# Kernel optimization log

Hardware: AMD Instinct MI355X
Metric: run time of the kernel (lower is better)

## Reference

```python
import jax, jax.numpy as jnp
import numpy as np

B, S, D = 2, 2048, 1024
H, KV, DH = 16, 4, 64
FI = 2816
V = 32000
NBLK = 2
NSTEPS = 3
CF = 0.67


def setup_inputs() -> dict:
    key = jax.random.key(0)
    ks = jax.random.split(key, 12)
    s = 0.02
    return {
        'input_ids': jax.random.randint(ks[0], (B, S), 0, V, dtype=jnp.int32),
        'emb': jax.random.normal(ks[1], (V, D), jnp.float32) * s,
        'Wq': jax.random.normal(ks[2], (NBLK, D, H * DH), jnp.float32) * s,
        'Wk': jax.random.normal(ks[3], (NBLK, D, KV * DH), jnp.float32) * s,
        'Wv': jax.random.normal(ks[4], (NBLK, D, KV * DH), jnp.float32) * s,
        'Wo': jax.random.normal(ks[5], (NBLK, H * DH, D), jnp.float32) * s,
        'Wg': jax.random.normal(ks[6], (NBLK, D, FI), jnp.float32) * s,
        'Wu': jax.random.normal(ks[7], (NBLK, D, FI), jnp.float32) * s,
        'Wd': jax.random.normal(ks[8], (NBLK, FI, D), jnp.float32) * s,
        'norm1': jnp.ones((NBLK, D), jnp.float32),
        'norm2': jnp.ones((NBLK, D), jnp.float32),
        'router_w': jax.random.normal(ks[9], (D, 1), jnp.float32) * s,
        'final_norm': jnp.ones((D,), jnp.float32),
        'lm_head': jax.random.normal(ks[10], (D, V), jnp.float32) * s,
    }


def rmsnorm(x, w, eps=1e-6):
    return x * jax.lax.rsqrt(jnp.mean(x * x, axis=-1, keepdims=True) + eps) * w


def rotate_half(x):
    x1, x2 = jnp.split(x, 2, axis=-1)
    return jnp.concatenate([-x2, x1], axis=-1)


def rope_tables(seq_len, dh):
    inv = 1.0 / (10000.0 ** (jnp.arange(0, dh, 2, dtype=jnp.float32) / dh))
    t = jnp.arange(seq_len, dtype=jnp.float32)
    freqs = t[:, None] * inv[None, :]                 # [S, dh/2]
    emb = jnp.concatenate([freqs, freqs], axis=-1)     # [S, dh]
    return jnp.cos(emb), jnp.sin(emb)


def shared_block(x, Wq, Wk, Wv, Wo, Wg, Wu, Wd, n1, n2):
    b, s, _ = x.shape
    h = rmsnorm(x, n1)
    q = (h @ Wq).reshape(b, s, H, DH).transpose(0, 2, 1, 3)   # bhsd
    k = (h @ Wk).reshape(b, s, KV, DH).transpose(0, 2, 1, 3)
    v = (h @ Wv).reshape(b, s, KV, DH).transpose(0, 2, 1, 3)
    cos, sin = rope_tables(s, DH)                              # [S, dh]
    q = q * cos + rotate_half(q) * sin
    k = k * cos + rotate_half(k) * sin
    k = jnp.repeat(k, H // KV, axis=1)   # repeat_interleave over head dim
    v = jnp.repeat(v, H // KV, axis=1)
    scale = 1.0 / jnp.sqrt(jnp.float32(DH))
    scores = jnp.einsum('bhqd,bhkd->bhqk', q, k) * scale
    causal = jnp.tril(jnp.ones((s, s), dtype=bool))
    scores = jnp.where(causal, scores, -jnp.inf)
    probs = jax.nn.softmax(scores, axis=-1)
    ctx = jnp.einsum('bhqk,bhkd->bhqd', probs, v)
    ctx = ctx.transpose(0, 2, 1, 3).reshape(b, s, H * DH)
    x = x + ctx @ Wo
    h2 = rmsnorm(x, n2)
    return x + (jax.nn.silu(h2 @ Wg) * (h2 @ Wu)) @ Wd


def reference(input_ids, emb, Wq, Wk, Wv, Wo, Wg, Wu, Wd, norm1, norm2,
              router_w, final_norm, lm_head):
    x = emb[input_ids]                      # [B, S, D]
    mask = jnp.ones((B, S), dtype=bool)     # all tokens active at depth 0
    aux_total = jnp.float32(0.0)
    n_active = B * S                        # static per step -> static top-k k
    for step in range(NSTEPS):
        keep = max(1, int(n_active * CF))
        if keep < n_active:
            # expert-choice router: sigmoid score, top-k over active tokens
            scores = jax.nn.sigmoid((x @ router_w)[..., 0])       # [B, S]
            flat = jnp.where(mask, scores, -jnp.inf).reshape(-1)  # [B*S]
            top_vals, top_idx = jax.lax.top_k(flat, keep)
            mask = jnp.zeros((B * S,), dtype=bool).at[top_idx].set(True).reshape(B, S)
            aux_total = aux_total + (-jnp.mean(top_vals) * 1e-3)
            n_active = keep
        blk = step % NBLK                   # 'cycle' sharing strategy
        out = shared_block(x, Wq[blk], Wk[blk], Wv[blk], Wo[blk],
                           Wg[blk], Wu[blk], Wd[blk], norm1[blk], norm2[blk])
        # only routed (active) tokens are updated at this recursion depth
        x = jnp.where(mask[..., None], out, x)
    x = rmsnorm(x, final_norm)
    logits = x @ lm_head                    # [B, S, V]
    return logits, aux_total
```

## Files before the change

### kernel.cpp

```cpp
#include <hip/hip_runtime.h>
#include <cmath>


constexpr int kB = 2, kS = 2048, kD = 1024, kH = 16, kKV = 4, kDH = 64,
              kFI = 2816, kV = 32000, kT = kB * kS;
constexpr size_t kBtOff  = 114688000;
constexpr size_t kAbfOff = 112590848;
constexpr size_t kXOff   = 108396544;
constexpr int kR1 = 3456;
constexpr int kQKV = 1536;
constexpr int kGU = 5632;

typedef __attribute__((ext_vector_type(8))) __bf16 bf16x8;
typedef __attribute__((ext_vector_type(4))) float f32x4;
typedef unsigned short u16;
typedef unsigned int u32;

__device__ inline u32 f2bf1(float f) {
  u32 u = __builtin_bit_cast(u32, f);
  return (u + 0x7FFFu + ((u >> 16) & 1u)) >> 16;
}
__device__ inline void splitbf(float v, u32& h, u32& l) {
  h = f2bf1(v);
  float hf = __builtin_bit_cast(float, h << 16);
  l = f2bf1(v - hf);
}
__device__ inline int xcd_remap(int hb, int nwg) {
  int q = nwg >> 3, r = nwg & 7;
  int xcd = hb & 7, pos = hb >> 3;
  int start = (xcd < r) ? xcd * (q + 1) : r * (q + 1) + (xcd - r) * q;
  return start + pos;
}

__device__ inline void stage_lds16(const u16* __restrict__ gbase, int K,
                                   int row0, int k0, char* ldsbase, int t) {
  int w = t >> 6, lane = t & 63;
#pragma unroll
  for (int i = 0; i < 4; ++i) {
    int wb = (w * 4 + i) * 1024;
    int L = wb + lane * 16;
    int r = L >> 7, inner = L & 127;
    int kc0 = (inner ^ ((r & 7) << 4)) >> 3;
    const u16* g = gbase + (size_t)(row0 + r) * K + k0 + kc0 * 4;
    __builtin_amdgcn_global_load_lds(
        (const __attribute__((address_space(1))) u32*)g,
        (__attribute__((address_space(3))) u32*)(ldsbase + wb), 16, 0, 0);
  }
}

__global__ __launch_bounds__(256) void tables_kernel(float* __restrict__ cosT,
                                                     float* __restrict__ sinT) {
  int tid = blockIdx.x * 256 + threadIdx.x;
  int t = tid >> 5, d = tid & 31;
  float inv = (float)pow(10000.0, -(double)d / 32.0);
  float fr = (float)t * inv;
  cosT[tid] = (float)cos((double)fr);
  sinT[tid] = (float)sin((double)fr);
}

__global__ void init_kernel(int* __restrict__ mask, float* __restrict__ aux) {
  int t = threadIdx.x;
  for (int e = t; e < kT; e += 256) mask[e] = 1;
  if (t == 0) aux[0] = 0.f;
}

__global__ __launch_bounds__(256) void embed_kernel(const int* __restrict__ ids,
    const float* __restrict__ emb, float* __restrict__ x) {
  int tid = blockIdx.x * 256 + threadIdx.x;
  int token = tid >> 8;
  int c4 = (tid & 255) << 2;
  int id = ids[token];
  *(float4*)&x[(size_t)token * kD + c4] =
      *(const float4*)&emb[(size_t)id * kD + c4];
}

__global__ __launch_bounds__(1024) void scan_kernel(const int* __restrict__ mask,
    int* __restrict__ cidx, int keep, int keepR) {
  __shared__ int sv[1024];
  int t = threadIdx.x;
  int base = t * 4;
  int loc[4];
  int c = 0;
#pragma unroll
  for (int j = 0; j < 4; ++j) { loc[j] = c; c += mask[base + j]; }
  sv[t] = c;
  __syncthreads();
  for (int off = 1; off < 1024; off <<= 1) {
    int v = (t >= off) ? sv[t - off] : 0;
    __syncthreads();
    sv[t] += v;
    __syncthreads();
  }
  int pre = (t == 0) ? 0 : sv[t - 1];
#pragma unroll
  for (int j = 0; j < 4; ++j)
    if (mask[base + j]) cidx[pre + loc[j]] = base + j;
  __syncthreads();
  for (int e = keep + t; e < keepR; e += 1024) cidx[e] = 0;
}

__global__ __launch_bounds__(256) void rmsnorm_split_kernel(
    const float* __restrict__ x, const float* __restrict__ w,
    u16* __restrict__ ohi, u16* __restrict__ olo) {
  int tok = blockIdx.x, t = threadIdx.x;
  const float* xr = x + (size_t)tok * kD;
  float4 xv = *(const float4*)&xr[t * 4];
  float s = xv.x * xv.x + xv.y * xv.y + xv.z * xv.z + xv.w * xv.w;
#pragma unroll
  for (int off = 1; off < 64; off <<= 1) s += __shfl_xor(s, off);
  __shared__ float red[4];
  if ((t & 63) == 0) red[t >> 6] = s;
  __syncthreads();
  float tot = red[0] + red[1] + red[2] + red[3];
  float sc = 1.f / sqrtf(tot * (1.f / kD) + 1e-6f);
  float4 wv = *(const float4*)&w[t * 4];
  float o0 = xv.x * sc * wv.x, o1 = xv.y * sc * wv.y;
  float o2 = xv.z * sc * wv.z, o3 = xv.w * sc * wv.w;
  u32 h0, h1, h2, h3, l0, l1, l2, l3;
  splitbf(o0, h0, l0); splitbf(o1, h1, l1);
  splitbf(o2, h2, l2); splitbf(o3, h3, l3);
  uint2 ph, pl;
  ph.x = h0 | (h1 << 16); ph.y = h2 | (h3 << 16);
  pl.x = l0 | (l1 << 16); pl.y = l2 | (l3 << 16);
  *(uint2*)&ohi[(size_t)tok * kD + t * 4] = ph;
  *(uint2*)&olo[(size_t)tok * kD + t * 4] = pl;
}

__global__ __launch_bounds__(256) void rmsnorm_split_gather(
    const float* __restrict__ x, const float* __restrict__ w,
    const int* __restrict__ cidx, u16* __restrict__ ohi, u16* __restrict__ olo) {
  int row = blockIdx.x, t = threadIdx.x;
  int tok = cidx[row];
  const float* xr = x + (size_t)tok * kD;
  float4 xv = *(const float4*)&xr[t * 4];
  float s = xv.x * xv.x + xv.y * xv.y + xv.z * xv.z + xv.w * xv.w;
#pragma unroll
  for (int off = 1; off < 64; off <<= 1) s += __shfl_xor(s, off);
  __shared__ float red[4];
  if ((t & 63) == 0) red[t >> 6] = s;
  __syncthreads();
  float tot = red[0] + red[1] + red[2] + red[3];
  float sc = 1.f / sqrtf(tot * (1.f / kD) + 1e-6f);
  float4 wv = *(const float4*)&w[t * 4];
  float o0 = xv.x * sc * wv.x, o1 = xv.y * sc * wv.y;
  float o2 = xv.z * sc * wv.z, o3 = xv.w * sc * wv.w;
  u32 h0, h1, h2, h3, l0, l1, l2, l3;
  splitbf(o0, h0, l0); splitbf(o1, h1, l1);
  splitbf(o2, h2, l2); splitbf(o3, h3, l3);
  uint2 ph, pl;
  ph.x = h0 | (h1 << 16); ph.y = h2 | (h3 << 16);
  pl.x = l0 | (l1 << 16); pl.y = l2 | (l3 << 16);
  *(uint2*)&ohi[(size_t)row * kD + t * 4] = ph;
  *(uint2*)&olo[(size_t)row * kD + t * 4] = pl;
}

__global__ __launch_bounds__(256) void finalnorm_conv(const float* __restrict__ x,
    const float* __restrict__ fnw, u16* __restrict__ Abf) {
  int tok = blockIdx.x, t = threadIdx.x;
  const float* xr = x + (size_t)tok * kD;
  float4 xv = *(const float4*)&xr[t * 4];
  float s = xv.x * xv.x + xv.y * xv.y + xv.z * xv.z + xv.w * xv.w;
#pragma unroll
  for (int off = 1; off < 64; off <<= 1) s += __shfl_xor(s, off);
  __shared__ float red[4];
  if ((t & 63) == 0) red[t >> 6] = s;
  __syncthreads();
  float tot = red[0] + red[1] + red[2] + red[3];
  float sc = 1.f / sqrtf(tot * (1.f / kD) + 1e-6f);
  float4 wv = *(const float4*)&fnw[t * 4];
  uint2 ph;
  ph.x = f2bf1(xv.x * sc * wv.x) | (f2bf1(xv.y * sc * wv.y) << 16);
  ph.y = f2bf1(xv.z * sc * wv.z) | (f2bf1(xv.w * sc * wv.w) << 16);
  *(uint2*)&Abf[(size_t)tok * kD + t * 4] = ph;
}

__global__ __launch_bounds__(64) void router_kernel(const float* __restrict__ x,
    const float* __restrict__ rw, float* __restrict__ scores) {
  int tok = blockIdx.x, lane = threadIdx.x;
  const float* xr = x + (size_t)tok * kD;
  double s = 0.0;
#pragma unroll
  for (int e = 0; e < kD / 64; ++e)
    s += (double)xr[lane + e * 64] * (double)rw[lane + e * 64];
#pragma unroll
  for (int off = 1; off < 64; off <<= 1) s += __shfl_xor(s, off);
  if (lane == 0) {
    float z = (float)s;
    scores[tok] = 1.f / (1.f + expf(-z));
  }
}

__global__ __launch_bounds__(1024) void topk_kernel(const float* __restrict__ scores,
    int* __restrict__ mask, float* __restrict__ aux, int keep) {
  __shared__ float sv[kT];
  __shared__ int si[kT];
  __shared__ float red[16];
  int t = threadIdx.x;
  for (int e = t; e < kT; e += 1024) {
    sv[e] = mask[e] ? scores[e] : -INFINITY;
    si[e] = e;
  }
  __syncthreads();
  for (int k = 2; k <= kT; k <<= 1) {
    for (int j = k >> 1; j > 0; j >>= 1) {
      for (int e = t; e < kT; e += 1024) {
        int p = e ^ j;
        if (p > e) {
          float v1 = sv[e], v2 = sv[p];
          int i1 = si[e], i2 = si[p];
          bool before = (v1 > v2) || (v1 == v2 && i1 < i2);
          bool desc = ((e & k) == 0);
          if (desc ? !before : before) {
            sv[e] = v2; sv[p] = v1; si[e] = i2; si[p] = i1;
          }
        }
      }
      __syncthreads();
    }
  }
  for (int e = t; e < kT; e += 1024) mask[si[e]] = (e < keep) ? 1 : 0;
  float ps = 0.f;
  for (int e = t; e < keep; e += 1024) ps += sv[e];
#pragma unroll
  for (int off = 1; off < 64; off <<= 1) ps += __shfl_xor(ps, off);
  if ((t & 63) == 0) red[t >> 6] = ps;
  __syncthreads();
  if (t == 0) {
    float tot = 0.f;
    for (int i = 0; i < 16; ++i) tot += red[i];
    aux[0] += -(tot / (float)keep) * 1e-3f;
  }
}

__global__ __launch_bounds__(256) void rope_split_kernel(
    const float* __restrict__ qkv,
    const float* __restrict__ cosT, const float* __restrict__ sinT,
    u16* __restrict__ Qh, u16* __restrict__ Ql,
    u16* __restrict__ Kh, u16* __restrict__ Kl) {
  int tid = blockIdx.x * 256 + threadIdx.x;
  const int QP = kT * kH * 32;
  const float* base;
  u16 *oh, *ol;
  size_t outoff;
  int token, d;
  if (tid < QP) {
    token = tid >> 9;
    int r = tid & 511;
    int hh = r >> 5; d = r & 31;
    base = qkv + (size_t)token * kQKV + hh * kDH;
    outoff = (size_t)token * (kH * kDH) + hh * kDH;
    oh = Qh; ol = Ql;
  } else {
    int p = tid - QP;
    token = p >> 7;
    int r = p & 127;
    int hh = r >> 5; d = r & 31;
    base = qkv + (size_t)token * kQKV + 1024 + hh * kDH;
    outoff = (size_t)token * (kKV * kDH) + hh * kDH;
    oh = Kh; ol = Kl;
  }
  int s = token & (kS - 1);
  float c = cosT[s * 32 + d], sn = sinT[s * 32 + d];
  float x1 = base[d], x2 = base[d + 32];
  float v1 = x1 * c - x2 * sn;
  float v2 = x2 * c + x1 * sn;
  u32 h1, l1, h2, l2;
  splitbf(v1, h1, l1);
  splitbf(v2, h2, l2);
  oh[outoff + d] = (u16)h1;      ol[outoff + d] = (u16)l1;
  oh[outoff + d + 32] = (u16)h2; ol[outoff + d + 32] = (u16)l2;
}

__global__ __launch_bounds__(256) void vtsplit_kernel(const float* __restrict__ qkv,
    u16* __restrict__ Th, u16* __restrict__ Tl) {
  int ktile = blockIdx.x, kv = blockIdx.y, b = blockIdx.z;
  __shared__ float T[64][65];
  int t = threadIdx.x;
#pragma unroll
  for (int p = 0; p < 16; ++p) {
    int idx = t + p * 256;
    int key = idx >> 6, d = idx & 63;
    T[key][d] =
        qkv[(size_t)(b * kS + ktile * 64 + key) * kQKV + 1280 + kv * kDH + d];
  }
  __syncthreads();
  int dr = t >> 2, kg = t & 3;
  size_t ob = ((size_t)(b * kKV + kv) * kDH + dr) * kS + ktile * 64 + kg * 16;
#pragma unroll
  for (int i = 0; i < 4; ++i) {
    int kk = kg * 16 + i * 4;
    u32 h0, h1, h2, h3, l0, l1, l2, l3;
    splitbf(T[kk + 0][dr], h0, l0); splitbf(T[kk + 1][dr], h1, l1);
    splitbf(T[kk + 2][dr], h2, l2); splitbf(T[kk + 3][dr], h3, l3);
    uint2 ph, pl;
    ph.x = h0 | (h1 << 16); ph.y = h2 | (h3 << 16);
    pl.x = l0 | (l1 << 16); pl.y = l2 | (l3 << 16);
    *(uint2*)&Th[ob + i * 4] = ph;
    *(uint2*)&Tl[ob + i * 4] = pl;
  }
}

__global__ __launch_bounds__(256) void attn_mfma(
    const u16* __restrict__ Qh, const u16* __restrict__ Ql,
    const u16* __restrict__ Kh2, const u16* __restrict__ Kl2,
    const u16* __restrict__ VTh, const u16* __restrict__ VTl,
    u16* __restrict__ ctxH, u16* __restrict__ ctxL) {
  int qb = (int)gridDim.x - 1 - (int)blockIdx.x;
  int q0 = qb * 64, hh = blockIdx.y, b = blockIdx.z;
  int t = threadIdx.x;
  int lane = t & 63, w = t >> 6;
  int kvh = hh >> 2;
  __shared__ __align__(16) char sQh[8192], sQl[8192];
  __shared__ __align__(16) char sKh[8192], sKl[8192];
  __shared__ __align__(16) char sVh[8192], sVl[8192];
  __shared__ __align__(16) char sPh[8192], sPl[8192];
#pragma unroll
  for (int p = 0; p < 4; ++p) {
    int idx = t + p * 256;
    int r = idx >> 4, kc = idx & 15;
    int off = r * 128 + ((kc * 8) ^ ((r & 7) << 4));
    size_t gq = (size_t)(b * kS + q0 + r) * (kH * kDH) + hh * kDH + kc * 4;
    *(uint2*)(sQh + off) = *(const uint2*)&Qh[gq];
    *(uint2*)(sQl + off) = *(const uint2*)&Ql[gq];
  }
  f32x4 ctxa[4];
#pragma unroll
  for (int i = 0; i < 4; ++i) ctxa[i] = {0.f, 0.f, 0.f, 0.f};
  float lsum[4] = {0.f, 0.f, 0.f, 0.f};
  int ntiles = qb + 1;
  for (int kt = 0; kt < ntiles; ++kt) {
    __syncthreads();
#pragma unroll
    for (int p = 0; p < 4; ++p) {
      int idx = t + p * 256;
      int r = idx >> 4, kc = idx & 15;
      int off = r * 128 + ((kc * 8) ^ ((r & 7) << 4));
      size_t gk = (size_t)(b * kS + kt * 64 + r) * (kKV * kDH) + kvh * kDH + kc * 4;
      size_t gv = ((size_t)(b * kKV + kvh) * kDH + r) * kS + kt * 64 + kc * 4;
      *(uint2*)(sKh + off) = *(const uint2*)&Kh2[gk];
      *(uint2*)(sKl + off) = *(const uint2*)&Kl2[gk];
      *(uint2*)(sVh + off) = *(const uint2*)&VTh[gv];
      *(uint2*)(sVl + off) = *(const uint2*)&VTl[gv];
    }
    __syncthreads();
    f32x4 sf[4];
#pragma unroll
    for (int i = 0; i < 4; ++i) sf[i] = {0.f, 0.f, 0.f, 0.f};
#pragma unroll
    for (int ks = 0; ks < 2; ++ks) {
      int m = w * 16 + (lane & 15);
      int kb = ks * 64 + ((lane >> 4) << 4);
      int ao = m * 128 + (kb ^ ((m & 7) << 4));
      bf16x8 qh8 = *(bf16x8*)(sQh + ao);
      bf16x8 ql8 = *(bf16x8*)(sQl + ao);
#pragma unroll
      for (int nf = 0; nf < 4; ++nf) {
        int n = nf * 16 + (lane & 15);
        int bo = n * 128 + (kb ^ ((n & 7) << 4));
        bf16x8 kh8 = *(bf16x8*)(sKh + bo);
        bf16x8 kl8 = *(bf16x8*)(sKl + bo);
        sf[nf] = __builtin_amdgcn_mfma_f32_16x16x32_bf16(qh8, kh8, sf[nf], 0, 0, 0);
        sf[nf] = __builtin_amdgcn_mfma_f32_16x16x32_bf16(qh8, kl8, sf[nf], 0, 0, 0);
        sf[nf] = __builtin_amdgcn_mfma_f32_16x16x32_bf16(ql8, kh8, sf[nf], 0, 0, 0);
      }
    }
    int qrow = (lane >> 4) << 2;
#pragma unroll
    for (int nf = 0; nf < 4; ++nf) {
      int key = kt * 64 + nf * 16 + (lane & 15);
#pragma unroll
      for (int rg = 0; rg < 4; ++rg) {
        int query = q0 + w * 16 + qrow + rg;
        float p = 0.f;
        if (key <= query) p = __expf(sf[nf][rg] * 0.125f);
        lsum[rg] += p;
        u32 ph, pl;
        splitbf(p, ph, pl);
        int ql_ = w * 16 + qrow + rg;
        int kl_ = nf * 16 + (lane & 15);
        int po = ql_ * 128 + ((kl_ * 2) ^ ((ql_ & 7) << 4));
        *(u16*)(sPh + po) = (u16)ph;
        *(u16*)(sPl + po) = (u16)pl;
      }
    }
#pragma unroll
    for (int ks = 0; ks < 2; ++ks) {
      int m = w * 16 + (lane & 15);
      int kb = ks * 64 + ((lane >> 4) << 4);
      int ao = m * 128 + (kb ^ ((m & 7) << 4));
      bf16x8 ph8 = *(bf16x8*)(sPh + ao);
      bf16x8 pl8 = *(bf16x8*)(sPl + ao);
#pragma unroll
      for (int nf = 0; nf < 4; ++nf) {
        int n = nf * 16 + (lane & 15);
        int bo = n * 128 + (kb ^ ((n & 7) << 4));
        bf16x8 vh8 = *(bf16x8*)(sVh + bo);
        bf16x8 vl8 = *(bf16x8*)(sVl + bo);
        ctxa[nf] = __builtin_amdgcn_mfma_f32_16x16x32_bf16(ph8, vh8, ctxa[nf], 0, 0, 0);
        ctxa[nf] = __builtin_amdgcn_mfma_f32_16x16x32_bf16(ph8, vl8, ctxa[nf], 0, 0, 0);
        ctxa[nf] = __builtin_amdgcn_mfma_f32_16x16x32_bf16(pl8, vh8, ctxa[nf], 0, 0, 0);
      }
    }
  }
#pragma unroll
  for (int rg = 0; rg < 4; ++rg) {
    float ps = lsum[rg];
    ps += __shfl_xor(ps, 1); ps += __shfl_xor(ps, 2);
    ps += __shfl_xor(ps, 4); ps += __shfl_xor(ps, 8);
    lsum[rg] = ps;
  }
#pragma unroll
  for (int nf = 0; nf < 4; ++nf) {
    int d = nf * 16 + (lane & 15);
#pragma unroll
    for (int rg = 0; rg < 4; ++rg) {
      int query = q0 + w * 16 + ((lane >> 4) << 2) + rg;
      float cv = ctxa[nf][rg] / lsum[rg];
      u32 ch, cl;
      splitbf(cv, ch, cl);
      size_t co = (size_t)(b * kS + query) * (kH * kDH) + hh * kDH + d;
      ctxH[co] = (u16)ch;
      ctxL[co] = (u16)cl;
    }
  }
}

__global__ __launch_bounds__(256) void silu_mul_split_kernel(
    const float* __restrict__ gu, u16* __restrict__ hi, u16* __restrict__ lo,
    int keepR) {
  int i = blockIdx.x * 256 + threadIdx.x;
  int total = keepR * (kFI / 4);
  if (i >= total) return;
  int row = i / (kFI / 4);
  int c4 = (i - row * (kFI / 4)) * 4;
  float4 gv = *(const float4*)&gu[(size_t)row * kGU + c4];
  float4 uv = *(const float4*)&gu[(size_t)row * kGU + kFI + c4];
  float m0 = (gv.x / (1.f + expf(-gv.x))) * uv.x;
  float m1 = (gv.y / (1.f + expf(-gv.y))) * uv.y;
  float m2 = (gv.z / (1.f + expf(-gv.z))) * uv.z;
  float m3 = (gv.w / (1.f + expf(-gv.w))) * uv.w;
  u32 h0, h1, h2, h3, l0, l1, l2, l3;
  splitbf(m0, h0, l0); splitbf(m1, h1, l1);
  splitbf(m2, h2, l2); splitbf(m3, h3, l3);
  uint2 ph, pl;
  ph.x = h0 | (h1 << 16); ph.y = h2 | (h3 << 16);
  pl.x = l0 | (l1 << 16); pl.y = l2 | (l3 << 16);
  *(uint2*)&hi[(size_t)row * kFI + c4] = ph;
  *(uint2*)&lo[(size_t)row * kFI + c4] = pl;
}

__global__ __launch_bounds__(256) void tsplit_kernel(const float* __restrict__ W,
    u16* __restrict__ Th, u16* __restrict__ Tl, int N, int K, size_t dstStride) {
  size_t mat = (size_t)blockIdx.z * (size_t)K * N;
  size_t dob = (size_t)blockIdx.z * dstStride;
  int n0 = blockIdx.x * 64, k0 = blockIdx.y * 64;
  __shared__ float T[64][65];
  int t = threadIdx.x;
#pragma unroll
  for (int p = 0; p < 16; ++p) {
    int idx = t + p * 256;
    int kl = idx >> 6, nl = idx & 63;
    T[nl][kl] = W[mat + (size_t)(k0 + kl) * N + n0 + nl];
  }
  __syncthreads();
  int nl = t >> 2, kg = t & 3;
  size_t ob = dob + (size_t)(n0 + nl) * K + k0 + kg * 16;
#pragma unroll
  for (int i = 0; i < 4; ++i) {
    int kk = kg * 16 + i * 4;
    u32 h0, h1, h2, h3, l0, l1, l2, l3;
    splitbf(T[nl][kk + 0], h0, l0); splitbf(T[nl][kk + 1], h1, l1);
    splitbf(T[nl][kk + 2], h2, l2); splitbf(T[nl][kk + 3], h3, l3);
    uint2 ph, pl;
    ph.x = h0 | (h1 << 16); ph.y = h2 | (h3 << 16);
    pl.x = l0 | (l1 << 16); pl.y = l2 | (l3 << 16);
    *(uint2*)&Th[ob + i * 4] = ph;
    *(uint2*)&Tl[ob + i * 4] = pl;
  }
}

__global__ __launch_bounds__(256) void tconv_kernel(const float* __restrict__ W,
    u16* __restrict__ Bt, int N, int K) {
  int n0 = blockIdx.x * 64, k0 = blockIdx.y * 64;
  __shared__ float T[64][65];
  int t = threadIdx.x;
#pragma unroll
  for (int p = 0; p < 16; ++p) {
    int idx = t + p * 256;
    int kl = idx >> 6, nl = idx & 63;
    T[nl][kl] = W[(size_t)(k0 + kl) * N + n0 + nl];
  }
  __syncthreads();
  int nl = t >> 2, kg = t & 3;
  size_t ob = (size_t)(n0 + nl) * K + k0 + kg * 16;
#pragma unroll
  for (int i = 0; i < 4; ++i) {
    int kk = kg * 16 + i * 4;
    uint2 ph;
    ph.x = f2bf1(T[nl][kk + 0]) | (f2bf1(T[nl][kk + 1]) << 16);
    ph.y = f2bf1(T[nl][kk + 2]) | (f2bf1(T[nl][kk + 3]) << 16);
    *(uint2*)&Bt[ob + i * 4] = ph;
  }
}

template <int MODE>
__global__ __launch_bounds__(256) void gemm_bf3(
    const u16* __restrict__ Ah, const u16* __restrict__ Al,
    const u16* __restrict__ Bh, const u16* __restrict__ Bl,
    float* __restrict__ C, int N, int K,
    const float* __restrict__ Add, const int* __restrict__ mask, int gridR,
    int keepM) {
  __shared__ __align__(16) char AsH[16384];
  __shared__ __align__(16) char AsL[16384];
  __shared__ __align__(16) char BsH[16384];
  __shared__ __align__(16) char BsL[16384];
  int t = threadIdx.x;
  int lane = t & 63, w = t >> 6;
  int wr = w >> 1, wc = w & 1;
  int lid = xcd_remap((int)blockIdx.x, (int)gridDim.x);
  int row0 = (lid % gridR) * 128, col0 = (lid / gridR) * 128;
  f32x4 acc[4][4];
#pragma unroll
  for (int i = 0; i < 4; ++i)
#pragma unroll
    for (int j = 0; j < 4; ++j) acc[i][j] = {0.f, 0.f, 0.f, 0.f};

  for (int k0 = 0; k0 < K; k0 += 64) {
    stage_lds16(Ah, K, row0, k0, AsH, t);
    stage_lds16(Al, K, row0, k0, AsL, t);
    stage_lds16(Bh, K, col0, k0, BsH, t);
    stage_lds16(Bl, K, col0, k0, BsL, t);
    __syncthreads();
#pragma unroll
    for (int ks = 0; ks < 2; ++ks) {
      bf16x8 ah[4], al4[4], bh[4], bl4[4];
      int kb = ks * 64 + ((lane >> 4) << 4);
#pragma unroll
      for (int i = 0; i < 4; ++i) {
        int m = wr * 64 + i * 16 + (lane & 15);
        int n = wc * 64 + i * 16 + (lane & 15);
        int ao = m * 128 + (kb ^ ((m & 7) << 4));
        int bo = n * 128 + (kb ^ ((n & 7) << 4));
        ah[i] = *(bf16x8*)(AsH + ao);
        al4[i] = *(bf16x8*)(AsL + ao);
        bh[i] = *(bf16x8*)(BsH + bo);
        bl4[i] = *(bf16x8*)(BsL + bo);
      }
#pragma unroll
      for (int mb = 0; mb < 4; ++mb)
#pragma unroll
        for (int nb = 0; nb < 4; ++nb) {
          acc[mb][nb] = __builtin_amdgcn_mfma_f32_16x16x32_bf16(
              ah[mb], bh[nb], acc[mb][nb], 0, 0, 0);
          acc[mb][nb] = __builtin_amdgcn_mfma_f32_16x16x32_bf16(
              ah[mb], bl4[nb], acc[mb][nb], 0, 0, 0);
          acc[mb][nb] = __builtin_amdgcn_mfma_f32_16x16x32_bf16(
              al4[mb], bh[nb], acc[mb][nb], 0, 0, 0);
        }
    }
    __syncthreads();
  }
#pragma unroll
  for (int mb = 0; mb < 4; ++mb) {
    int rb = row0 + wr * 64 + mb * 16 + ((lane >> 4) << 2);
#pragma unroll
    for (int rg = 0; rg < 4; ++rg) {
      int r = rb + rg;
      if (MODE == 2 && !mask[r]) continue;
      if (MODE == 3 && r >= keepM) continue;
      int ro = (MODE == 3) ? mask[r] : r;
#pragma unroll
      for (int nb = 0; nb < 4; ++nb) {
        int c = col0 + wc * 64 + nb * 16 + (lane & 15);
        float vv = acc[mb][nb][rg];
        if (MODE >= 1) vv += Add[(size_t)ro * N + c];
        C[(size_t)ro * N + c] = vv;
      }
    }
  }
}

__global__ __launch_bounds__(256) void lmhead_fast(const u16* __restrict__ Abf,
    const u16* __restrict__ Bt, float* __restrict__ C, int N, int K, int gridR) {
  __shared__ __align__(16) char AsB[16384];
  __shared__ __align__(16) char BsB[16384];
  int t = threadIdx.x;
  int lane = t & 63, w = t >> 6;
  int wr = w >> 1, wc = w & 1;
  int lid = xcd_remap((int)blockIdx.x, (int)gridDim.x);
  int panels = (int)gridDim.x / gridR;
  const int RG = 14;
  int fullg = gridR / RG;
  int lastr = gridR - fullg * RG;
  int fgb = fullg * RG * panels;
  int row, panel;
  if (lid < fgb) {
    int g = lid / (RG * panels);
    int r2 = lid % (RG * panels);
    row = g * RG + (r2 % RG);
    panel = r2 / RG;
  } else {
    int r2 = lid - fgb;
    row = fullg * RG + (r2 % lastr);
    panel = r2 / lastr;
  }
  int row0 = row * 128, col0 = panel * 128;
  f32x4 acc[4][4];
#pragma unroll
  for (int i = 0; i < 4; ++i)
#pragma unroll
    for (int j = 0; j < 4; ++j) acc[i][j] = {0.f, 0.f, 0.f, 0.f};

  for (int k0 = 0; k0 < K; k0 += 64) {
    stage_lds16(Abf, K, row0, k0, AsB, t);
    stage_lds16(Bt, K, col0, k0, BsB, t);
    __syncthreads();
#pragma unroll
    for (int ks = 0; ks < 2; ++ks) {
      bf16x8 af[4], bfr[4];
      int kb = ks * 64 + ((lane >> 4) << 4);
#pragma unroll
      for (int i = 0; i < 4; ++i) {
        int m = wr * 64 + i * 16 + (lane & 15);
        int n = wc * 64 + i * 16 + (lane & 15);
        af[i] = *(bf16x8*)(AsB + m * 128 + (kb ^ ((m & 7) << 4)));
        bfr[i] = *(bf16x8*)(BsB + n * 128 + (kb ^ ((n & 7) << 4)));
      }
#pragma unroll
      for (int mb = 0; mb < 4; ++mb)
#pragma unroll
        for (int nb = 0; nb < 4; ++nb)
          acc[mb][nb] = __builtin_amdgcn_mfma_f32_16x16x32_bf16(
              af[mb], bfr[nb], acc[mb][nb], 0, 0, 0);
    }
    __syncthreads();
  }
#pragma unroll
  for (int mb = 0; mb < 4; ++mb) {
    int row2 = row0 + wr * 64 + mb * 16 + ((lane >> 4) << 2);
#pragma unroll
    for (int nb = 0; nb < 4; ++nb) {
      int col = col0 + wc * 64 + nb * 16 + (lane & 15);
#pragma unroll
      for (int rg = 0; rg < 4; ++rg)
        __builtin_nontemporal_store(acc[mb][nb][rg],
                                    &C[(size_t)(row2 + rg) * N + col]);
    }
  }
}

__global__ __launch_bounds__(256) void lmhead_hyb(const u16* __restrict__ Abf2,
    const float* __restrict__ Bm, float* __restrict__ C, int N, int K, int gridR) {
  __shared__ __align__(16) char AsB[16384];
  __shared__ __align__(16) char BsB[16384];
  __shared__ float sBf[64][132];
  int t = threadIdx.x;
  int lane = t & 63, w = t >> 6;
  int wr = w >> 1, wc = w & 1;
  int lid = xcd_remap((int)blockIdx.x, (int)gridDim.x);
  int row0 = (lid % gridR) * 128, col0 = (lid / gridR) * 128;
  f32x4 acc[4][4];
#pragma unroll
  for (int i = 0; i < 4; ++i)
#pragma unroll
    for (int j = 0; j < 4; ++j) acc[i][j] = {0.f, 0.f, 0.f, 0.f};

  for (int k0 = 0; k0 < K; k0 += 64) {
    stage_lds16(Abf2, K, row0, k0, AsB, t);
#pragma unroll
    for (int p = 0; p < 8; ++p) {
      int idx = t + p * 256;
      int kk = idx >> 5, c4 = (idx & 31) << 2;
      *(float4*)&sBf[kk][c4] = *(const float4*)&Bm[(size_t)(k0 + kk) * N + col0 + c4];
    }
    __syncthreads();
#pragma unroll
    for (int p = 0; p < 4; ++p) {
      int nl = t & 127;
      int kb = ((t >> 7) << 3) + p * 16;
      unsigned pk[4];
#pragma unroll
      for (int j = 0; j < 4; ++j)
        pk[j] = f2bf1(sBf[kb + 2 * j][nl]) | (f2bf1(sBf[kb + 2 * j + 1][nl]) << 16);
      uint4 w4; w4.x = pk[0]; w4.y = pk[1]; w4.z = pk[2]; w4.w = pk[3];
      *(uint4*)(BsB + nl * 128 + ((kb * 2) ^ ((nl & 7) << 4))) = w4;
    }
    __syncthreads();
#pragma unroll
    for (int ks = 0; ks < 2; ++ks) {
      bf16x8 af[4], bfr[4];
      int kb = ks * 64 + ((lane >> 4) << 4);
#pragma unroll
      for (int i = 0; i < 4; ++i) {
        int m = wr * 64 + i * 16 + (lane & 15);
        int n = wc * 64 + i * 16 + (lane & 15);
        af[i] = *(bf16x8*)(AsB + m * 128 + (kb ^ ((m & 7) << 4)));
        bfr[i] = *(bf16x8*)(BsB + n * 128 + (kb ^ ((n & 7) << 4)));
      }
#pragma unroll
      for (int mb = 0; mb < 4; ++mb)
#pragma unroll
        for (int nb = 0; nb < 4; ++nb)
          acc[mb][nb] = __builtin_amdgcn_mfma_f32_16x16x32_bf16(
              af[mb], bfr[nb], acc[mb][nb], 0, 0, 0);
    }
    __syncthreads();
  }
#pragma unroll
  for (int mb = 0; mb < 4; ++mb) {
    int row = row0 + wr * 64 + mb * 16 + ((lane >> 4) << 2);
#pragma unroll
    for (int nb = 0; nb < 4; ++nb) {
      int col = col0 + wc * 64 + nb * 16 + (lane & 15);
#pragma unroll
      for (int rg = 0; rg < 4; ++rg)
        __builtin_nontemporal_store(acc[mb][nb][rg],
                                    &C[(size_t)(row + rg) * N + col]);
    }
  }
}

__global__ __launch_bounds__(256) void copy_kernel(const float* __restrict__ src,
    float* __restrict__ dst, int n) {
  int i = blockIdx.x * 256 + threadIdx.x;
  if (i < n) dst[i] = src[i];
}

__global__ void finish_kernel(const float* __restrict__ aux, float* __restrict__ dst) {
  dst[0] = aux[0];
}

extern "C" void kernel_launch(void* const* d_in, const int* in_sizes, int n_in,
                              void* d_out, int out_size, void* d_ws, size_t ws_size,
                              hipStream_t stream) {
  const int* ids = (const int*)d_in[0];
  const float* emb = (const float*)d_in[1];
  const float* Wq = (const float*)d_in[2];
  const float* Wk = (const float*)d_in[3];
  const float* Wv = (const float*)d_in[4];
  const float* Wo = (const float*)d_in[5];
  const float* Wg = (const float*)d_in[6];
  const float* Wu = (const float*)d_in[7];
  const float* Wd = (const float*)d_in[8];
  const float* n1 = (const float*)d_in[9];
  const float* n2 = (const float*)d_in[10];
  const float* rw = (const float*)d_in[11];
  const float* fn = (const float*)d_in[12];
  const float* lmh = (const float*)d_in[13];
  float* out = (float*)d_out;

  float* ws = (float*)d_ws;
  size_t woff = 0;
  float* cosT = ws + woff;   woff += (size_t)kS * 32;
  float* sinT = ws + woff;   woff += (size_t)kS * 32;
  float* scores = ws + woff; woff += kT;
  float* aux = ws + woff;    woff += 4;
  int* mask = (int*)(ws + woff); woff += kT;
  int* cidx = (int*)(ws + woff); woff += kT;
  u16* Abf2 = (u16*)(ws + woff);

  float* x = out + kXOff;
  u16* Abf = (u16*)(out + kAbfOff);
  u16* Bt = (u16*)(out + kBtOff);
  size_t off = 0;
  auto alloc = [&](size_t n) { float* p = out + off; off += n; return p; };
  float* qkv  = alloc((size_t)kT * kQKV);
  float* xa   = alloc((size_t)kT * kD);
  float* gu   = alloc((size_t)kT * kGU);
  u16* hH   = (u16*)alloc((size_t)kT * kD / 2);
  u16* hL   = (u16*)alloc((size_t)kT * kD / 2);
  u16* ctxH = (u16*)alloc((size_t)kT * kD / 2);
  u16* ctxL = (u16*)alloc((size_t)kT * kD / 2);
  u16* mmH  = (u16*)alloc((size_t)kT * kFI / 2);
  u16* mmL  = (u16*)alloc((size_t)kT * kFI / 2);
  u16* QhB  = (u16*)alloc((size_t)kT * kH * kDH / 2);
  u16* QlB  = (u16*)alloc((size_t)kT * kH * kDH / 2);
  u16* KhB  = (u16*)alloc((size_t)kT * kKV * kDH / 2);
  u16* KlB  = (u16*)alloc((size_t)kT * kKV * kDH / 2);
  u16* VTh  = (u16*)alloc((size_t)kT * kKV * kDH / 2);
  u16* VTl  = (u16*)alloc((size_t)kT * kKV * kDH / 2);
  u16* WqkvH = (u16*)alloc(1572864); u16* WqkvL = (u16*)alloc(1572864);
  u16* WoH   = (u16*)alloc(1048576); u16* WoL   = (u16*)alloc(1048576);
  u16* WguH  = (u16*)alloc(5767168); u16* WguL  = (u16*)alloc(5767168);
  u16* WdH   = (u16*)alloc(2883584); u16* WdL   = (u16*)alloc(2883584);
  (void)in_sizes; (void)n_in; (void)ws_size;

  tables_kernel<<<kS * 32 / 256, 256, 0, stream>>>(cosT, sinT);
  init_kernel<<<1, 256, 0, stream>>>(mask, aux);
  embed_kernel<<<kT, 256, 0, stream>>>(ids, emb, x);

  const size_t sQKV = (size_t)kQKV * kD;
  const size_t sGU = (size_t)kGU * kD;
  tsplit_kernel<<<dim3(16, 16, 2), 256, 0, stream>>>(
      Wq, WqkvH, WqkvL, 1024, 1024, sQKV);
  tsplit_kernel<<<dim3(4, 16, 2), 256, 0, stream>>>(
      Wk, WqkvH + 1024 * 1024, WqkvL + 1024 * 1024, 256, 1024, sQKV);
  tsplit_kernel<<<dim3(4, 16, 2), 256, 0, stream>>>(
      Wv, WqkvH + 1280 * 1024, WqkvL + 1280 * 1024, 256, 1024, sQKV);
  tsplit_kernel<<<dim3(16, 16, 2), 256, 0, stream>>>(
      Wo, WoH, WoL, 1024, 1024, (size_t)1024 * 1024);
  tsplit_kernel<<<dim3(44, 16, 2), 256, 0, stream>>>(
      Wg, WguH, WguL, 2816, 1024, sGU);
  tsplit_kernel<<<dim3(44, 16, 2), 256, 0, stream>>>(
      Wu, WguH + 2816 * 1024, WguL + 2816 * 1024, 2816, 1024, sGU);
  tsplit_kernel<<<dim3(16, 44, 2), 256, 0, stream>>>(
      Wd, WdH, WdL, 1024, 2816, (size_t)2816 * 1024);
  tconv_kernel<<<dim3(kV / 64, kD / 64), 256, 0, stream>>>(lmh, Bt, kV, kD);

  const int keeps[3] = {2744, 1838, 1231};
  const int tiles[3] = {22, 15, 10};
  for (int step = 0; step < 3; ++step) {
    int blk = step % 2;
    int keep = keeps[step], nt = tiles[step], keepR = nt * 128;
    size_t qkvo = (size_t)blk * sQKV;
    size_t oo = (size_t)blk * (kH * kDH) * kD;
    size_t guo = (size_t)blk * sGU;
    size_t dofs = (size_t)blk * kFI * kD;
    router_kernel<<<kT, 64, 0, stream>>>(x, rw, scores);
    topk_kernel<<<1, 1024, 0, stream>>>(scores, mask, aux, keep);
    scan_kernel<<<1, 1024, 0, stream>>>(mask, cidx, keep, keepR);
    rmsnorm_split_kernel<<<kT, 256, 0, stream>>>(x, n1 + (size_t)blk * kD, hH, hL);
    gemm_bf3<0><<<32 * 12, 256, 0, stream>>>(
        hH, hL, WqkvH + qkvo, WqkvL + qkvo, qkv, kQKV, kD, nullptr, nullptr, 32, 0);
    rope_split_kernel<<<(kT * kH * 32 + kT * kKV * 32) / 256, 256, 0, stream>>>(
        qkv, cosT, sinT, QhB, QlB, KhB, KlB);
    vtsplit_kernel<<<dim3(kS / 64, kKV, kB), 256, 0, stream>>>(qkv, VTh, VTl);
    attn_mfma<<<dim3(kS / 64, kH, kB), 256, 0, stream>>>(
        QhB, QlB, KhB, KlB, VTh, VTl, ctxH, ctxL);
    gemm_bf3<1><<<32 * 8, 256, 0, stream>>>(
        ctxH, ctxL, WoH + oo, WoL + oo, xa, kD, kH * kDH, x, nullptr, 32, 0);
    rmsnorm_split_gather<<<keepR, 256, 0, stream>>>(
        xa, n2 + (size_t)blk * kD, cidx, hH, hL);
    gemm_bf3<0><<<nt * 44, 256, 0, stream>>>(
        hH, hL, WguH + guo, WguL + guo, gu, kGU, kD, nullptr, nullptr, nt, 0);
    silu_mul_split_kernel<<<(keepR * (kFI / 4) + 255) / 256, 256, 0, stream>>>(
        gu, mmH, mmL, keepR);
    gemm_bf3<3><<<nt * 8, 256, 0, stream>>>(
        mmH, mmL, WdH + dofs, WdL + dofs, x, kD, kFI, xa, cidx, nt, keep);
  }

  finalnorm_conv<<<kT, 256, 0, stream>>>(x, fn, Abf);
  copy_kernel<<<(kT - kR1) * kD / 2 / 256, 256, 0, stream>>>(
      (const float*)(Abf + (size_t)kR1 * kD), (float*)Abf2, (kT - kR1) * kD / 2);
  lmhead_fast<<<(kR1 / 128) * (kV / 128), 256, 0, stream>>>(
      Abf, Bt, out, kV, kD, kR1 / 128);
  lmhead_hyb<<<((kT - kR1) / 128) * (kV / 128), 256, 0, stream>>>(
      Abf2, lmh, out + (size_t)kR1 * kV, kV, kD, (kT - kR1) / 128);
  finish_kernel<<<1, 1, 0, stream>>>(aux, out + (size_t)out_size - 1);
}
```

Baseline: 2.278 ms.

## Compute attention and Wo projection only for routed tokens via compacted index list

The scan now builds a per-batch compacted token list, padding each batch segment to a multiple of 64 by repeating the last token. Attention runs only over query blocks drawn from this list, and the Wo GEMM writes compacted rows, so the second rmsnorm no longer gathers. This skips attention and output-projection work for tokens the router dropped, and causal tiles are bounded by the last token in each block. In exchange the scan kernel is more complex, padded duplicate rows do redundant writes, and scattered Q loads replace contiguous ones.

```diff
diff --git a/kernel.cpp b/kernel.cpp
--- a/kernel.cpp
+++ b/kernel.cpp
@@ -74,29 +74,45 @@
       *(const float4*)&emb[(size_t)id * kD + c4];
 }
 
-__global__ __launch_bounds__(1024) void scan_kernel(const int* __restrict__ mask,
-    int* __restrict__ cidx, int keep, int keepR) {
+__global__ __launch_bounds__(1024) void scan2_kernel(const int* __restrict__ mask,
+    int* __restrict__ cidx2, int keepR2) {
   __shared__ int sv[1024];
-  int t = threadIdx.x;
-  int base = t * 4;
-  int loc[4];
-  int c = 0;
-#pragma unroll
-  for (int j = 0; j < 4; ++j) { loc[j] = c; c += mask[base + j]; }
-  sv[t] = c;
-  __syncthreads();
-  for (int off = 1; off < 1024; off <<= 1) {
-    int v = (t >= off) ? sv[t - off] : 0;
-    __syncthreads();
-    sv[t] += v;
-    __syncthreads();
-  }
-  int pre = (t == 0) ? 0 : sv[t - 1];
-#pragma unroll
-  for (int j = 0; j < 4; ++j)
-    if (mask[base + j]) cidx[pre + loc[j]] = base + j;
-  __syncthreads();
-  for (int e = keep + t; e < keepR; e += 1024) cidx[e] = 0;
+  __shared__ int slist[2944];
+  __shared__ int padlen_s;
+  int t = threadIdx.x;
+  if (t == 0) padlen_s = 0;
+  __syncthreads();
+  for (int b = 0; b < 2; ++b) {
+    int base = b * 2048;
+    int m0 = mask[base + t * 2], m1 = mask[base + t * 2 + 1];
+    sv[t] = m0 + m1;
+    __syncthreads();
+    for (int off = 1; off < 1024; off <<= 1) {
+      int v = (t >= off) ? sv[t - off] : 0;
+      __syncthreads();
+      sv[t] += v;
+      __syncthreads();
+    }
+    int pre = (t == 0) ? 0 : sv[t - 1];
+    int cb = sv[1023];
+    int seg = padlen_s;
+    if (m0) slist[seg + pre] = base + t * 2;
+    if (m1) slist[seg + pre + m0] = base + t * 2 + 1;
+    __syncthreads();
+    int padded = ((cb + 63) >> 6) << 6;
+    if (cb > 0) {
+      int last = slist[seg + cb - 1];
+      for (int e = cb + t; e < padded; e += 1024) slist[seg + e] = last;
+    }
+    __syncthreads();
+    if (t == 0) padlen_s = seg + padded;
+    __syncthreads();
+  }
+  int pl = padlen_s;
+  int lastAll = slist[pl - 1];
+  for (int e = pl + t; e < keepR2; e += 1024) slist[e] = lastAll;
+  __syncthreads();
+  for (int e = t; e < keepR2; e += 1024) cidx2[e] = slist[e];
 }
 
 __global__ __launch_bounds__(256) void rmsnorm_split_kernel(
@@ -124,34 +140,6 @@
   pl.x = l0 | (l1 << 16); pl.y = l2 | (l3 << 16);
   *(uint2*)&ohi[(size_t)tok * kD + t * 4] = ph;
   *(uint2*)&olo[(size_t)tok * kD + t * 4] = pl;
-}
-
-__global__ __launch_bounds__(256) void rmsnorm_split_gather(
-    const float* __restrict__ x, const float* __restrict__ w,
-    const int* __restrict__ cidx, u16* __restrict__ ohi, u16* __restrict__ olo) {
-  int row = blockIdx.x, t = threadIdx.x;
-  int tok = cidx[row];
-  const float* xr = x + (size_t)tok * kD;
-  float4 xv = *(const float4*)&xr[t * 4];
-  float s = xv.x * xv.x + xv.y * xv.y + xv.z * xv.z + xv.w * xv.w;
-#pragma unroll
-  for (int off = 1; off < 64; off <<= 1) s += __shfl_xor(s, off);
-  __shared__ float red[4];
-  if ((t & 63) == 0) red[t >> 6] = s;
-  __syncthreads();
-  float tot = red[0] + red[1] + red[2] + red[3];
-  float sc = 1.f / sqrtf(tot * (1.f / kD) + 1e-6f);
-  float4 wv = *(const float4*)&w[t * 4];
-  float o0 = xv.x * sc * wv.x, o1 = xv.y * sc * wv.y;
-  float o2 = xv.z * sc * wv.z, o3 = xv.w * sc * wv.w;
-  u32 h0, h1, h2, h3, l0, l1, l2, l3;
-  splitbf(o0, h0, l0); splitbf(o1, h1, l1);
-  splitbf(o2, h2, l2); splitbf(o3, h3, l3);
-  uint2 ph, pl;
-  ph.x = h0 | (h1 << 16); ph.y = h2 | (h3 << 16);
-  pl.x = l0 | (l1 << 16); pl.y = l2 | (l3 << 16);
-  *(uint2*)&ohi[(size_t)row * kD + t * 4] = ph;
-  *(uint2*)&olo[(size_t)row * kD + t * 4] = pl;
 }
 
 __global__ __launch_bounds__(256) void finalnorm_conv(const float* __restrict__ x,
@@ -304,9 +292,10 @@
     const u16* __restrict__ Qh, const u16* __restrict__ Ql,
     const u16* __restrict__ Kh2, const u16* __restrict__ Kl2,
     const u16* __restrict__ VTh, const u16* __restrict__ VTl,
+    const int* __restrict__ cidx2,
     u16* __restrict__ ctxH, u16* __restrict__ ctxL) {
-  int qb = (int)gridDim.x - 1 - (int)blockIdx.x;
-  int q0 = qb * 64, hh = blockIdx.y, b = blockIdx.z;
+  int blk = (int)gridDim.x - 1 - (int)blockIdx.x;
+  int q0c = blk * 64, hh = blockIdx.y;
   int t = threadIdx.x;
   int lane = t & 63, w = t >> 6;
   int kvh = hh >> 2;
@@ -314,12 +303,17 @@
   __shared__ __align__(16) char sKh[8192], sKl[8192];
   __shared__ __align__(16) char sVh[8192], sVl[8192];
   __shared__ __align__(16) char sPh[8192], sPl[8192];
+  __shared__ int sTok[64];
+  if (t < 64) sTok[t] = cidx2[q0c + t];
+  __syncthreads();
+  int b = sTok[0] >> 11;
+  int ntiles = ((sTok[63] & (kS - 1)) >> 6) + 1;
 #pragma unroll
   for (int p = 0; p < 4; ++p) {
     int idx = t + p * 256;
     int r = idx >> 4, kc = idx & 15;
     int off = r * 128 + ((kc * 8) ^ ((r & 7) << 4));
-    size_t gq = (size_t)(b * kS + q0 + r) * (kH * kDH) + hh * kDH + kc * 4;
+    size_t gq = (size_t)sTok[r] * (kH * kDH) + hh * kDH + kc * 4;
     *(uint2*)(sQh + off) = *(const uint2*)&Qh[gq];
     *(uint2*)(sQl + off) = *(const uint2*)&Ql[gq];
   }
@@ -327,7 +321,6 @@
 #pragma unroll
   for (int i = 0; i < 4; ++i) ctxa[i] = {0.f, 0.f, 0.f, 0.f};
   float lsum[4] = {0.f, 0.f, 0.f, 0.f};
-  int ntiles = qb + 1;
   for (int kt = 0; kt < ntiles; ++kt) {
     __syncthreads();
 #pragma unroll
@@ -365,14 +358,16 @@
       }
     }
     int qrow = (lane >> 4) << 2;
+    int qp[4];
+#pragma unroll
+    for (int rg = 0; rg < 4; ++rg) qp[rg] = sTok[w * 16 + qrow + rg] & (kS - 1);
 #pragma unroll
     for (int nf = 0; nf < 4; ++nf) {
       int key = kt * 64 + nf * 16 + (lane & 15);
 #pragma unroll
       for (int rg = 0; rg < 4; ++rg) {
-        int query = q0 + w * 16 + qrow + rg;
         float p = 0.f;
-        if (key <= query) p = __expf(sf[nf][rg] * 0.125f);
+        if (key <= qp[rg]) p = __expf(sf[nf][rg] * 0.125f);
         lsum[rg] += p;
         u32 ph, pl;
         splitbf(p, ph, pl);
@@ -414,11 +409,11 @@
     int d = nf * 16 + (lane & 15);
 #pragma unroll
     for (int rg = 0; rg < 4; ++rg) {
-      int query = q0 + w * 16 + ((lane >> 4) << 2) + rg;
+      int crow = q0c + w * 16 + ((lane >> 4) << 2) + rg;
       float cv = ctxa[nf][rg] / lsum[rg];
       u32 ch, cl;
       splitbf(cv, ch, cl);
-      size_t co = (size_t)(b * kS + query) * (kH * kDH) + hh * kDH + d;
+      size_t co = (size_t)crow * (kH * kDH) + hh * kDH + d;
       ctxH[co] = (u16)ch;
       ctxL[co] = (u16)cl;
     }
@@ -508,8 +503,7 @@
     const u16* __restrict__ Ah, const u16* __restrict__ Al,
     const u16* __restrict__ Bh, const u16* __restrict__ Bl,
     float* __restrict__ C, int N, int K,
-    const float* __restrict__ Add, const int* __restrict__ mask, int gridR,
-    int keepM) {
+    const float* __restrict__ Add, const int* __restrict__ mask, int gridR) {
   __shared__ __align__(16) char AsH[16384];
   __shared__ __align__(16) char AsL[16384];
   __shared__ __align__(16) char BsH[16384];
@@ -566,15 +560,16 @@
 #pragma unroll
     for (int rg = 0; rg < 4; ++rg) {
       int r = rb + rg;
-      if (MODE == 2 && !mask[r]) continue;
-      if (MODE == 3 && r >= keepM) continue;
-      int ro = (MODE == 3) ? mask[r] : r;
+      int wrow = r, arow = r;
+      if (MODE == 3) wrow = mask[r];
+      if (MODE == 4) arow = mask[r];
 #pragma unroll
       for (int nb = 0; nb < 4; ++nb) {
         int c = col0 + wc * 64 + nb * 16 + (lane & 15);
         float vv = acc[mb][nb][rg];
-        if (MODE >= 1) vv += Add[(size_t)ro * N + c];
-        C[(size_t)ro * N + c] = vv;
+        if (MODE == 3) vv += Add[(size_t)r * N + c];
+        if (MODE == 4) vv += Add[(size_t)arow * N + c];
+        C[(size_t)wrow * N + c] = vv;
       }
     }
   }
@@ -756,7 +751,7 @@
   float* scores = ws + woff; woff += kT;
   float* aux = ws + woff;    woff += 4;
   int* mask = (int*)(ws + woff); woff += kT;
-  int* cidx = (int*)(ws + woff); woff += kT;
+  int* cidx2 = (int*)(ws + woff); woff += kT;
   u16* Abf2 = (u16*)(ws + woff);
 
   float* x = out + kXOff;
@@ -807,36 +802,38 @@
       Wd, WdH, WdL, 1024, 2816, (size_t)2816 * 1024);
   tconv_kernel<<<dim3(kV / 64, kD / 64), 256, 0, stream>>>(lmh, Bt, kV, kD);
 
-  const int keeps[3] = {2744, 1838, 1231};
-  const int tiles[3] = {22, 15, 10};
+  const int keeps[3]  = {2744, 1838, 1231};
+  const int keepR2[3] = {2944, 2048, 1408};
+  const int nt2[3]    = {23, 16, 11};
   for (int step = 0; step < 3; ++step) {
     int blk = step % 2;
-    int keep = keeps[step], nt = tiles[step], keepR = nt * 128;
+    int keep = keeps[step], kr2 = keepR2[step], nt = nt2[step];
+    int ablocks = kr2 / 64;
     size_t qkvo = (size_t)blk * sQKV;
     size_t oo = (size_t)blk * (kH * kDH) * kD;
     size_t guo = (size_t)blk * sGU;
     size_t dofs = (size_t)blk * kFI * kD;
     router_kernel<<<kT, 64, 0, stream>>>(x, rw, scores);
     topk_kernel<<<1, 1024, 0, stream>>>(scores, mask, aux, keep);
-    scan_kernel<<<1, 1024, 0, stream>>>(mask, cidx, keep, keepR);
+    scan2_kernel<<<1, 1024, 0, stream>>>(mask, cidx2, kr2);
     rmsnorm_split_kernel<<<kT, 256, 0, stream>>>(x, n1 + (size_t)blk * kD, hH, hL);
     gemm_bf3<0><<<32 * 12, 256, 0, stream>>>(
-        hH, hL, WqkvH + qkvo, WqkvL + qkvo, qkv, kQKV, kD, nullptr, nullptr, 32, 0);
+        hH, hL, WqkvH + qkvo, WqkvL + qkvo, qkv, kQKV, kD, nullptr, nullptr, 32);
     rope_split_kernel<<<(kT * kH * 32 + kT * kKV * 32) / 256, 256, 0, stream>>>(
         qkv, cosT, sinT, QhB, QlB, KhB, KlB);
     vtsplit_kernel<<<dim3(kS / 64, kKV, kB), 256, 0, stream>>>(qkv, VTh, VTl);
-    attn_mfma<<<dim3(kS / 64, kH, kB), 256, 0, stream>>>(
-        QhB, QlB, KhB, KlB, VTh, VTl, ctxH, ctxL);
-    gemm_bf3<1><<<32 * 8, 256, 0, stream>>>(
-        ctxH, ctxL, WoH + oo, WoL + oo, xa, kD, kH * kDH, x, nullptr, 32, 0);
-    rmsnorm_split_gather<<<keepR, 256, 0, stream>>>(
-        xa, n2 + (size_t)blk * kD, cidx, hH, hL);
+    attn_mfma<<<dim3(ablocks, kH), 256, 0, stream>>>(
+        QhB, QlB, KhB, KlB, VTh, VTl, cidx2, ctxH, ctxL);
+    gemm_bf3<4><<<nt * 8, 256, 0, stream>>>(
+        ctxH, ctxL, WoH + oo, WoL + oo, xa, kD, kH * kDH, x, cidx2, nt);
+    rmsnorm_split_kernel<<<kr2, 256, 0, stream>>>(
+        xa, n2 + (size_t)blk * kD, hH, hL);
     gemm_bf3<0><<<nt * 44, 256, 0, stream>>>(
-        hH, hL, WguH + guo, WguL + guo, gu, kGU, kD, nullptr, nullptr, nt, 0);
-    silu_mul_split_kernel<<<(keepR * (kFI / 4) + 255) / 256, 256, 0, stream>>>(
-        gu, mmH, mmL, keepR);
+        hH, hL, WguH + guo, WguL + guo, gu, kGU, kD, nullptr, nullptr, nt);
+    silu_mul_split_kernel<<<(kr2 * (kFI / 4) + 255) / 256, 256, 0, stream>>>(
+        gu, mmH, mmL, kr2);
     gemm_bf3<3><<<nt * 8, 256, 0, stream>>>(
-        mmH, mmL, WdH + dofs, WdL + dofs, x, kD, kFI, xa, cidx, nt, keep);
+        mmH, mmL, WdH + dofs, WdL + dofs, x, kD, kFI, xa, cidx2, nt);
   }
 
   finalnorm_conv<<<kT, 256, 0, stream>>>(x, fn, Abf);
```

New measurement: 2.042 ms. 10.4% less time.
